# Kernel tuning notes

Hardware: AMD Instinct MI355X
Metric: run time of the kernel (lower is better)

## Reference

```python
import jax, jax.numpy as jnp
import numpy as np

EMBED_DIM = 1024
HEAD_DIM = 64


def setup_inputs() -> dict:
    key = jax.random.key(0)
    ks = jax.random.split(key, 7)
    B, S = 4, 2048
    s = 1.0 / np.sqrt(EMBED_DIM)
    h = jax.random.normal(ks[0], (B, S, EMBED_DIM), dtype=jnp.float32)
    Wq = jax.random.normal(ks[1], (EMBED_DIM, HEAD_DIM), dtype=jnp.float32) * s
    bq = jax.random.normal(ks[2], (HEAD_DIM,), dtype=jnp.float32) * 0.01
    Wk = jax.random.normal(ks[3], (EMBED_DIM, HEAD_DIM), dtype=jnp.float32) * s
    bk = jax.random.normal(ks[4], (HEAD_DIM,), dtype=jnp.float32) * 0.01
    Wv = jax.random.normal(ks[5], (EMBED_DIM, HEAD_DIM), dtype=jnp.float32) * s
    bv = jax.random.normal(ks[6], (HEAD_DIM,), dtype=jnp.float32) * 0.01
    return {"h": h, "Wq": Wq, "bq": bq, "Wk": Wk, "bk": bk, "Wv": Wv, "bv": bv}


def reference(h, Wq, bq, Wk, bk, Wv, bv):
    # Linear projections: h [B,S,E] -> q,k [B,S,D]
    q = jnp.einsum("bse,ed->bsd", h, Wq) + bq
    k = jnp.einsum("bse,ed->bsd", h, Wk) + bk
    v = jnp.einsum("bse,ed->bsd", h, Wv) + bv  # computed but UNUSED (faithful to source)
    del v
    scale = 1.0 / jnp.sqrt(jnp.asarray(HEAD_DIM, dtype=q.dtype))
    # scores [B, Sq, Sk]
    scores = jnp.einsum("bqd,bkd->bqk", q, k) * scale
    # NOTE: source uses softmax over dim=1 (query axis), not the key axis
    weights = jax.nn.softmax(scores, axis=1)
    # NOTE: source passes h (not v) as the value tensor
    out = jnp.einsum("bqk,bke->bqe", weights, h)  # [B, Sq, E]
    return out
```

## Files before the change

### kernel.cpp

```cpp
#include <hip/hip_runtime.h>
#include <hip/hip_bf16.h>
#include <math.h>

#define EMBED 1024
#define HDIM  64
#define BATCH 4
#define SEQ   2048

typedef __attribute__((ext_vector_type(8))) short short8;
typedef __attribute__((ext_vector_type(4))) float f32x4;
typedef unsigned int u32;
typedef unsigned short u16;

static __device__ __forceinline__ u16 f2bf(float f) {
    union { float f; u32 u; } v; v.f = f;
    u32 r = v.u + 0x7fffu + ((v.u >> 16) & 1u);
    return (u16)(r >> 16);
}

static __device__ __forceinline__ void gload_lds16(const u16* g, u16* l) {
    __builtin_amdgcn_global_load_lds(
        (const __attribute__((address_space(1))) u32*)g,
        (__attribute__((address_space(3))) u32*)l, 16, 0, 0);
}

__global__ __launch_bounds__(256) void wt_kernel(
    const float* __restrict__ Wq, const float* __restrict__ Wk,
    u16* __restrict__ WqT, u16* __restrict__ WkT)
{
    __shared__ float tile[64][65];
    const float* W = blockIdx.y ? Wk : Wq;
    u16* WT = blockIdx.y ? WkT : WqT;
    int e0 = blockIdx.x * 64;
    int t = threadIdx.x, c = t & 63, r4 = t >> 6;
    for (int r = r4; r < 64; r += 4)
        tile[r][c] = W[(size_t)(e0 + r) * HDIM + c];
    __syncthreads();
    for (int d = r4; d < 64; d += 4)
        WT[(size_t)d * EMBED + e0 + c] = f2bf(tile[c][d]);
}

__global__ __launch_bounds__(256) void proj_kernel(
    const float* __restrict__ h, const u16* __restrict__ WqT, const u16* __restrict__ WkT,
    const float* __restrict__ bq, const float* __restrict__ bk,
    u16* __restrict__ Qbf, u16* __restrict__ Kbf)
{
    __shared__ u16 hs[2][16][136];
    int b = blockIdx.x >> 7, s0 = (blockIdx.x & 127) * 16;
    int t = threadIdx.x, lane = t & 63, w = t >> 6;
    int l15 = lane & 15, quad = lane >> 4;
    int pj = w >> 1, nh = (w & 1) * 32;
    const float* hb = h + ((size_t)b * SEQ + s0) * EMBED;
    const u16* Wp = pj ? WkT : WqT;
    int r = t >> 4, c4 = (t & 15) * 4;

    f32x4 preA0 = *(const f32x4*)(hb + (size_t)r * EMBED + c4);
    f32x4 preA1 = *(const f32x4*)(hb + (size_t)r * EMBED + 64 + c4);
    f32x4 preB0 = *(const f32x4*)(hb + (size_t)r * EMBED + 128 + c4);
    f32x4 preB1 = *(const f32x4*)(hb + (size_t)r * EMBED + 192 + c4);
    f32x4 accA[2], accB[2];
    accA[0] = accA[1] = accB[0] = accB[1] = (f32x4){0.f, 0.f, 0.f, 0.f};

    const u16* Wrow0 = Wp + (size_t)(nh + l15) * EMBED;
    const u16* Wrow1 = Wp + (size_t)(nh + 16 + l15) * EMBED;

    short8 cw[8];
#pragma unroll
    for (int i = 0; i < 4; i++) {
        cw[i]     = *(const short8*)(Wrow0 + i * 32 + quad * 8);
        cw[4 + i] = *(const short8*)(Wrow1 + i * 32 + quad * 8);
    }

    for (int it = 0; it < 8; ++it) {
        int ec = it * 128, buf = it & 1;
        uint2 pk;
        pk.x = (u32)f2bf(preA0[0]) | ((u32)f2bf(preA0[1]) << 16);
        pk.y = (u32)f2bf(preA0[2]) | ((u32)f2bf(preA0[3]) << 16);
        *(uint2*)&hs[buf][r][c4] = pk;
        pk.x = (u32)f2bf(preA1[0]) | ((u32)f2bf(preA1[1]) << 16);
        pk.y = (u32)f2bf(preA1[2]) | ((u32)f2bf(preA1[3]) << 16);
        *(uint2*)&hs[buf][r][64 + c4] = pk;
        __syncthreads();

        preA0 = preB0; preA1 = preB1;
        if (it + 2 < 8) {
            preB0 = *(const f32x4*)(hb + (size_t)r * EMBED + ec + 256 + c4);
            preB1 = *(const f32x4*)(hb + (size_t)r * EMBED + ec + 320 + c4);
        }
        short8 nw[8];
#pragma unroll
        for (int i = 0; i < 8; i++) nw[i] = cw[i];
        if (it + 1 < 8) {
#pragma unroll
            for (int i = 0; i < 4; i++) {
                nw[i]     = *(const short8*)(Wrow0 + ec + 128 + i * 32 + quad * 8);
                nw[4 + i] = *(const short8*)(Wrow1 + ec + 128 + i * 32 + quad * 8);
            }
        }

        short8 a0 = *(const short8*)&hs[buf][l15][quad * 8];
        short8 a1 = *(const short8*)&hs[buf][l15][32 + quad * 8];
        short8 a2 = *(const short8*)&hs[buf][l15][64 + quad * 8];
        short8 a3 = *(const short8*)&hs[buf][l15][96 + quad * 8];
        accA[0] = __builtin_amdgcn_mfma_f32_16x16x32_bf16(a0, cw[0], accA[0], 0, 0, 0);
        accA[1] = __builtin_amdgcn_mfma_f32_16x16x32_bf16(a0, cw[4], accA[1], 0, 0, 0);
        accB[0] = __builtin_amdgcn_mfma_f32_16x16x32_bf16(a1, cw[1], accB[0], 0, 0, 0);
        accB[1] = __builtin_amdgcn_mfma_f32_16x16x32_bf16(a1, cw[5], accB[1], 0, 0, 0);
        accA[0] = __builtin_amdgcn_mfma_f32_16x16x32_bf16(a2, cw[2], accA[0], 0, 0, 0);
        accA[1] = __builtin_amdgcn_mfma_f32_16x16x32_bf16(a2, cw[6], accA[1], 0, 0, 0);
        accB[0] = __builtin_amdgcn_mfma_f32_16x16x32_bf16(a3, cw[3], accB[0], 0, 0, 0);
        accB[1] = __builtin_amdgcn_mfma_f32_16x16x32_bf16(a3, cw[7], accB[1], 0, 0, 0);
#pragma unroll
        for (int i = 0; i < 8; i++) cw[i] = nw[i];
    }

    const float* bias = pj ? bk : bq;
    float scale = pj ? 1.0f : 0.125f;
    u16* outp = pj ? Kbf : Qbf;
    float bv0 = bias[nh + l15], bv1 = bias[nh + 16 + l15];
#pragma unroll
    for (int rr = 0; rr < 4; rr++) {
        size_t row = (size_t)b * SEQ + s0 + quad * 4 + rr;
        outp[row * HDIM + nh + l15]      = f2bf((accA[0][rr] + accB[0][rr] + bv0) * scale);
        outp[row * HDIM + nh + 16 + l15] = f2bf((accA[1][rr] + accB[1][rr] + bv1) * scale);
    }
}

__global__ __launch_bounds__(512) void sw_kernel(
    const u16* __restrict__ Qbf, const u16* __restrict__ Kbf,
    u16* __restrict__ Wmat, float* __restrict__ invl)
{
    __shared__ float sl[8][64];
    int b = blockIdx.y;
    int k0 = blockIdx.x * 64;
    int t = threadIdx.x, lane = t & 63, w = t >> 6;
    int l15 = lane & 15, quad = lane >> 4;
    const u16* Qb = Qbf + (size_t)b * SEQ * HDIM;
    const u16* Kb = Kbf + (size_t)b * SEQ * HDIM;
    u16* Wb = Wmat + (size_t)b * SEQ * SEQ;

    short8 kfr[4][2];
#pragma unroll
    for (int g = 0; g < 4; g++)
#pragma unroll
        for (int hh = 0; hh < 2; hh++)
            kfr[g][hh] = *(const short8*)(
                Kb + (size_t)(k0 + g * 16 + l15) * HDIM + hh * 32 + quad * 8);

    f32x4 lacc[4];
#pragma unroll
    for (int g = 0; g < 4; g++) lacc[g] = (f32x4){0.f, 0.f, 0.f, 0.f};

    int qs = w * 256;
    short8 cf[2][2];
#pragma unroll
    for (int a = 0; a < 2; a++)
#pragma unroll
        for (int hh = 0; hh < 2; hh++)
            cf[a][hh] = *(const short8*)(
                Qb + (size_t)(qs + a * 16 + l15) * HDIM + hh * 32 + quad * 8);

    for (int q0 = qs; q0 < qs + 256; q0 += 32) {
        short8 nf[2][2];
#pragma unroll
        for (int a = 0; a < 2; a++)
#pragma unroll
            for (int hh = 0; hh < 2; hh++) nf[a][hh] = cf[a][hh];
        if (q0 + 32 < qs + 256) {
#pragma unroll
            for (int a = 0; a < 2; a++)
#pragma unroll
                for (int hh = 0; hh < 2; hh++)
                    nf[a][hh] = *(const short8*)(
                        Qb + (size_t)(q0 + 32 + a * 16 + l15) * HDIM + hh * 32 + quad * 8);
        }
        f32x4 acc[2][4];
#pragma unroll
        for (int a = 0; a < 2; a++)
#pragma unroll
            for (int g = 0; g < 4; g++) acc[a][g] = (f32x4){0.f, 0.f, 0.f, 0.f};
#pragma unroll
        for (int a = 0; a < 2; a++)
#pragma unroll
            for (int g = 0; g < 4; g++) {
                acc[a][g] = __builtin_amdgcn_mfma_f32_16x16x32_bf16(
                    kfr[g][0], cf[a][0], acc[a][g], 0, 0, 0);
                acc[a][g] = __builtin_amdgcn_mfma_f32_16x16x32_bf16(
                    kfr[g][1], cf[a][1], acc[a][g], 0, 0, 0);
            }
#pragma unroll
        for (int a = 0; a < 2; a++) {
            u16* wrow = Wb + (size_t)(q0 + a * 16 + l15) * SEQ + k0;
#pragma unroll
            for (int g = 0; g < 4; g++) {
                float e0 = __expf(acc[a][g][0]), e1 = __expf(acc[a][g][1]);
                float e2 = __expf(acc[a][g][2]), e3 = __expf(acc[a][g][3]);
                lacc[g][0] += e0; lacc[g][1] += e1;
                lacc[g][2] += e2; lacc[g][3] += e3;
                uint2 pk;
                pk.x = (u32)f2bf(e0) | ((u32)f2bf(e1) << 16);
                pk.y = (u32)f2bf(e2) | ((u32)f2bf(e3) << 16);
                *(uint2*)(wrow + g * 16 + quad * 4) = pk;
            }
        }
#pragma unroll
        for (int a = 0; a < 2; a++)
#pragma unroll
            for (int hh = 0; hh < 2; hh++) cf[a][hh] = nf[a][hh];
    }
#pragma unroll
    for (int m = 1; m <= 8; m <<= 1)
#pragma unroll
        for (int g = 0; g < 4; g++) {
            lacc[g][0] += __shfl_xor(lacc[g][0], m, 64);
            lacc[g][1] += __shfl_xor(lacc[g][1], m, 64);
            lacc[g][2] += __shfl_xor(lacc[g][2], m, 64);
            lacc[g][3] += __shfl_xor(lacc[g][3], m, 64);
        }
    if (l15 == 0) {
#pragma unroll
        for (int g = 0; g < 4; g++) {
            sl[w][g * 16 + quad * 4 + 0] = lacc[g][0];
            sl[w][g * 16 + quad * 4 + 1] = lacc[g][1];
            sl[w][g * 16 + quad * 4 + 2] = lacc[g][2];
            sl[w][g * 16 + quad * 4 + 3] = lacc[g][3];
        }
    }
    __syncthreads();
    if (t < 64) {
        float s = ((sl[0][t] + sl[1][t]) + (sl[2][t] + sl[3][t]))
                + ((sl[4][t] + sl[5][t]) + (sl[6][t] + sl[7][t]));
        invl[b * SEQ + k0 + t] = 1.0f / s;
    }
}

__global__ __launch_bounds__(256) void tscale_kernel(
    const float* __restrict__ h, const float* __restrict__ invl,
    u16* __restrict__ hT)
{
    __shared__ float tile[64][65];
    int b  = blockIdx.z;
    int s0 = blockIdx.x * 64, e0 = blockIdx.y * 64;
    int t = threadIdx.x;
    int r16 = t >> 4, c4 = (t & 15) * 4;
    const float* hb = h + (size_t)b * SEQ * EMBED;
#pragma unroll
    for (int rr = r16; rr < 64; rr += 16) {
        f32x4 v = *(const f32x4*)(hb + (size_t)(s0 + rr) * EMBED + e0 + c4);
        *(f32x4*)&tile[rr][c4] = v;
    }
    __syncthreads();
    f32x4 il4 = *(const f32x4*)(invl + b * SEQ + s0 + c4);
    u16* hTb = hT + (size_t)b * EMBED * SEQ;
#pragma unroll
    for (int er = r16; er < 64; er += 16) {
        u16 p0 = f2bf(tile[c4 + 0][er] * il4[0]);
        u16 p1 = f2bf(tile[c4 + 1][er] * il4[1]);
        u16 p2 = f2bf(tile[c4 + 2][er] * il4[2]);
        u16 p3 = f2bf(tile[c4 + 3][er] * il4[3]);
        uint2 pk;
        pk.x = (u32)p0 | ((u32)p1 << 16);
        pk.y = (u32)p2 | ((u32)p3 << 16);
        *(uint2*)(hTb + (size_t)(e0 + er) * SEQ + s0 + c4) = pk;
    }
}

__global__ __launch_bounds__(512, 2) void out_gemm_kernel(
    const u16* __restrict__ Wmat, const u16* __restrict__ hT, float* __restrict__ out)
{
    __shared__ __align__(16) char smem[3 * 49152];
    int b = blockIdx.z;
    int q0 = blockIdx.x * 256, e0 = blockIdx.y * 128;
    int t = threadIdx.x, lane = t & 63, w = t >> 6;
    int l15 = lane & 15, quad = lane >> 4;
    const u16* Wb  = Wmat + (size_t)b * SEQ * SEQ;
    const u16* hTb = hT + (size_t)b * EMBED * SEQ;
    int kf = w >> 2;
    int wm = (w >> 1) & 1, wn = w & 1;
    int wq = wm * 128, we = wn * 64;

    f32x4 acc[8][4];
#pragma unroll
    for (int i = 0; i < 8; i++)
#pragma unroll
        for (int j = 0; j < 4; j++) acc[i][j] = (f32x4){0.f, 0.f, 0.f, 0.f};

    int st_rl = lane >> 3;
    int st_pc = lane & 7;

    const u16* gA[4];
    const u16* gB[2];
#pragma unroll
    for (int ld = 0; ld < 4; ld++) {
        int row = w * 32 + ld * 8 + st_rl;
        int cg  = st_pc ^ (row & 7);
        gA[ld] = Wb + (size_t)(q0 + row) * SEQ + cg * 8;
    }
#pragma unroll
    for (int ld = 0; ld < 2; ld++) {
        int row = w * 16 + ld * 8 + st_rl;
        int cg  = st_pc ^ (row & 7);
        gB[ld] = hTb + (size_t)(e0 + row) * SEQ + cg * 8;
    }
    int dA[4], dB[2];
#pragma unroll
    for (int ld = 0; ld < 4; ld++) dA[ld] = (w * 32 + ld * 8) * 128 + lane * 16;
#pragma unroll
    for (int ld = 0; ld < 2; ld++) dB[ld] = 32768 + (w * 16 + ld * 8) * 128 + lane * 16;
    int offA[8], offB[4];
#pragma unroll
    for (int ii = 0; ii < 8; ii++) {
        int ra  = wq + ii * 16 + l15;
        int pca = (kf * 4 + quad) ^ (ra & 7);
        offA[ii] = ra * 128 + pca * 16;
    }
#pragma unroll
    for (int j = 0; j < 4; j++) {
        int rb  = we + j * 16 + l15;
        int pcb = (kf * 4 + quad) ^ (rb & 7);
        offB[j] = 32768 + rb * 128 + pcb * 16;
    }

#define STAGE_H1(si)                                                           \
    {                                                                          \
        gload_lds16(gA[0], (u16*)(smem + (si) * 49152 + dA[0]));               \
        gload_lds16(gA[1], (u16*)(smem + (si) * 49152 + dA[1]));               \
        gload_lds16(gB[0], (u16*)(smem + (si) * 49152 + dB[0]));               \
    }
#define STAGE_H2(si)                                                           \
    {                                                                          \
        gload_lds16(gA[2], (u16*)(smem + (si) * 49152 + dA[2]));               \
        gload_lds16(gA[3], (u16*)(smem + (si) * 49152 + dA[3]));               \
        gload_lds16(gB[1], (u16*)(smem + (si) * 49152 + dB[1]));               \
    }
#define ADV()                                                                  \
    {                                                                          \
        gA[0] += 64; gA[1] += 64; gA[2] += 64; gA[3] += 64;                    \
        gB[0] += 64; gB[1] += 64;                                              \
    }

#define MFMA16(i0)                                                             \
    {                                                                          \
        _Pragma("unroll")                                                      \
        for (int ii = 0; ii < 4; ii++)                                         \
            _Pragma("unroll")                                                  \
            for (int j = 0; j < 4; j++)                                        \
                acc[(i0) + ii][j] = __builtin_amdgcn_mfma_f32_16x16x32_bf16(   \
                    af[ii], bfr[j], acc[(i0) + ii][j], 0, 0, 0);               \
    }

#define TILE(si, si2, DO_STAGE, VMC)                                           \
    {                                                                          \
        const char* Sb = smem + (si) * 49152;                                  \
        short8 af[4], bfr[4];                                                  \
                                                                  \
        _Pragma("unroll")                                                      \
        for (int ii = 0; ii < 4; ii++)                                         \
            af[ii] = *(const short8*)(Sb + offA[ii]);                          \
        _Pragma("unroll")                                                      \
        for (int j = 0; j < 4; j++)                                            \
            bfr[j] = *(const short8*)(Sb + offB[j]);                           \
        if (DO_STAGE) STAGE_H1(si2)                                            \
        __builtin_amdgcn_s_barrier();                                          \
        asm volatile("s_waitcnt lgkmcnt(0)" ::: "memory");                     \
        __builtin_amdgcn_sched_barrier(0);                                     \
        __builtin_amdgcn_s_setprio(1);                                         \
        MFMA16(0)                                                              \
        __builtin_amdgcn_s_setprio(0);                                         \
        __builtin_amdgcn_s_barrier();                                          \
                                                                  \
        _Pragma("unroll")                                                      \
        for (int ii = 0; ii < 4; ii++)                                         \
            af[ii] = *(const short8*)(Sb + offA[4 + ii]);                      \
        if (DO_STAGE) { STAGE_H2(si2) ADV() }                                  \
        __builtin_amdgcn_s_barrier();                                          \
        asm volatile("s_waitcnt lgkmcnt(0)" ::: "memory");                     \
        __builtin_amdgcn_sched_barrier(0);                                     \
        __builtin_amdgcn_s_setprio(1);                                         \
        MFMA16(4)                                                              \
        __builtin_amdgcn_s_setprio(0);                                         \
        if ((VMC) == 6) { asm volatile("s_waitcnt vmcnt(6)" ::: "memory"); }   \
        else if ((VMC) == 0) { asm volatile("s_waitcnt vmcnt(0)" ::: "memory"); } \
        __builtin_amdgcn_s_barrier();                                          \
    }

    STAGE_H1(0) STAGE_H2(0) ADV()
    STAGE_H1(1) STAGE_H2(1) ADV()
    asm volatile("s_waitcnt vmcnt(6)" ::: "memory");
    __builtin_amdgcn_s_barrier();

    for (int g = 0; g < 10; ++g) {
        TILE(0, 2, true, 6)
        TILE(1, 0, true, 6)
        TILE(2, 1, true, 6)
    }
    TILE(0, 2, false, 0)
    TILE(1, 0, false, -1)
#undef TILE
#undef STAGE_H1
#undef STAGE_H2
#undef ADV
#undef MFMA16

    float* red = (float*)smem;
    if (w >= 4) {
        float* reg = red + (size_t)(w & 3) * 8192;
#pragma unroll
        for (int i = 0; i < 8; i++)
#pragma unroll
            for (int j = 0; j < 4; j++)
                *(f32x4*)(reg + ((i * 4 + j) * 64 + lane) * 4) = acc[i][j];
    }
    __syncthreads();
    if (w < 4) {
        float* reg = red + (size_t)w * 8192;
        float* outb = out + (size_t)b * SEQ * EMBED;
#pragma unroll
        for (int i = 0; i < 8; i++)
#pragma unroll
            for (int j = 0; j < 4; j++) {
                f32x4 o = *(const f32x4*)(reg + ((i * 4 + j) * 64 + lane) * 4);
                o += acc[i][j];
#pragma unroll
                for (int r = 0; r < 4; r++)
                    outb[(size_t)(q0 + wq + i * 16 + quad * 4 + r) * EMBED
                         + e0 + we + j * 16 + l15] = o[r];
            }
    }
}

extern "C" void kernel_launch(void* const* d_in, const int* in_sizes, int n_in,
                              void* d_out, int out_size, void* d_ws, size_t ws_size,
                              hipStream_t stream) {
    (void)in_sizes; (void)n_in; (void)out_size; (void)ws_size;
    const float* h  = (const float*)d_in[0];
    const float* Wq = (const float*)d_in[1];
    const float* bq = (const float*)d_in[2];
    const float* Wk = (const float*)d_in[3];
    const float* bk = (const float*)d_in[4];
    float* out = (float*)d_out;

    char* ws = (char*)d_ws;
    u16*   Qbf  = (u16*)(ws);
    u16*   Kbf  = (u16*)(ws + (1ull << 20));
    u16*   hT   = (u16*)(ws + (2ull << 20));
    float* invl = (float*)(ws + (18ull << 20));
    u16*   WqT  = (u16*)(ws + (18ull << 20) + (128ull << 10));
    u16*   WkT  = (u16*)(ws + (18ull << 20) + (256ull << 10));
    u16*   Wmat = (u16*)(ws + (19ull << 20));

    hipLaunchKernelGGL(wt_kernel, dim3(16, 2), dim3(256), 0, stream, Wq, Wk, WqT, WkT);
    hipLaunchKernelGGL(proj_kernel, dim3(512), dim3(256), 0, stream,
                       h, WqT, WkT, bq, bk, Qbf, Kbf);
    hipLaunchKernelGGL(sw_kernel, dim3(32, 4), dim3(512), 0, stream,
                       Qbf, Kbf, Wmat, invl);
    hipLaunchKernelGGL(tscale_kernel, dim3(32, 16, 4), dim3(256), 0, stream,
                       h, invl, hT);
    hipLaunchKernelGGL(out_gemm_kernel, dim3(8, 8, 4), dim3(512), 0, stream,
                       Wmat, hT, out);
}
```

Baseline: 177.6 us.

## Split score-softmax kernel across query chunks with atomic column-sum reduction

The sw_kernel grid grows from 128 to 512 blocks by giving each block a quarter of the query range. Per-key exp sums are now combined across blocks with global atomicAdd into a buffer that wt_kernel zeroes first, and tscale_kernel takes the reciprocal itself. This targets under-occupancy: the old 128-block grid with long serial loops left most of the GPU's CUs idle. In exchange it adds atomic traffic, drops the Q-fragment prefetch, and makes the float summation order nondeterministic.

```diff
diff --git a/kernel.cpp b/kernel.cpp
--- a/kernel.cpp
+++ b/kernel.cpp
@@ -26,13 +26,14 @@
 
 __global__ __launch_bounds__(256) void wt_kernel(
     const float* __restrict__ Wq, const float* __restrict__ Wk,
-    u16* __restrict__ WqT, u16* __restrict__ WkT)
+    u16* __restrict__ WqT, u16* __restrict__ WkT, float* __restrict__ lsum)
 {
     __shared__ float tile[64][65];
     const float* W = blockIdx.y ? Wk : Wq;
     u16* WT = blockIdx.y ? WkT : WqT;
     int e0 = blockIdx.x * 64;
     int t = threadIdx.x, c = t & 63, r4 = t >> 6;
+    lsum[(blockIdx.y * 16 + blockIdx.x) * 256 + t] = 0.f;
     for (int r = r4; r < 64; r += 4)
         tile[r][c] = W[(size_t)(e0 + r) * HDIM + c];
     __syncthreads();
@@ -128,10 +129,9 @@
 
 __global__ __launch_bounds__(512) void sw_kernel(
     const u16* __restrict__ Qbf, const u16* __restrict__ Kbf,
-    u16* __restrict__ Wmat, float* __restrict__ invl)
+    u16* __restrict__ Wmat, float* __restrict__ lsum)
 {
-    __shared__ float sl[8][64];
-    int b = blockIdx.y;
+    int b = blockIdx.z;
     int k0 = blockIdx.x * 64;
     int t = threadIdx.x, lane = t & 63, w = t >> 6;
     int l15 = lane & 15, quad = lane >> 4;
@@ -151,29 +151,19 @@
 #pragma unroll
     for (int g = 0; g < 4; g++) lacc[g] = (f32x4){0.f, 0.f, 0.f, 0.f};
 
-    int qs = w * 256;
-    short8 cf[2][2];
-#pragma unroll
-    for (int a = 0; a < 2; a++)
-#pragma unroll
-        for (int hh = 0; hh < 2; hh++)
-            cf[a][hh] = *(const short8*)(
-                Qb + (size_t)(qs + a * 16 + l15) * HDIM + hh * 32 + quad * 8);
-
-    for (int q0 = qs; q0 < qs + 256; q0 += 32) {
-        short8 nf[2][2];
+    int qs = (blockIdx.y * 8 + w) * 64;
+
+#pragma unroll
+    for (int half = 0; half < 2; ++half) {
+        int q0 = qs + half * 32;
+        short8 cf[2][2];
 #pragma unroll
         for (int a = 0; a < 2; a++)
 #pragma unroll
-            for (int hh = 0; hh < 2; hh++) nf[a][hh] = cf[a][hh];
-        if (q0 + 32 < qs + 256) {
-#pragma unroll
-            for (int a = 0; a < 2; a++)
-#pragma unroll
-                for (int hh = 0; hh < 2; hh++)
-                    nf[a][hh] = *(const short8*)(
-                        Qb + (size_t)(q0 + 32 + a * 16 + l15) * HDIM + hh * 32 + quad * 8);
-        }
+            for (int hh = 0; hh < 2; hh++)
+                cf[a][hh] = *(const short8*)(
+                    Qb + (size_t)(q0 + a * 16 + l15) * HDIM + hh * 32 + quad * 8);
+
         f32x4 acc[2][4];
 #pragma unroll
         for (int a = 0; a < 2; a++)
@@ -203,10 +193,6 @@
                 *(uint2*)(wrow + g * 16 + quad * 4) = pk;
             }
         }
-#pragma unroll
-        for (int a = 0; a < 2; a++)
-#pragma unroll
-            for (int hh = 0; hh < 2; hh++) cf[a][hh] = nf[a][hh];
     }
 #pragma unroll
     for (int m = 1; m <= 8; m <<= 1)
@@ -218,24 +204,19 @@
             lacc[g][3] += __shfl_xor(lacc[g][3], m, 64);
         }
     if (l15 == 0) {
+        float* lp = lsum + b * SEQ + k0 + quad * 4;
 #pragma unroll
         for (int g = 0; g < 4; g++) {
-            sl[w][g * 16 + quad * 4 + 0] = lacc[g][0];
-            sl[w][g * 16 + quad * 4 + 1] = lacc[g][1];
-            sl[w][g * 16 + quad * 4 + 2] = lacc[g][2];
-            sl[w][g * 16 + quad * 4 + 3] = lacc[g][3];
+            atomicAdd(lp + g * 16 + 0, lacc[g][0]);
+            atomicAdd(lp + g * 16 + 1, lacc[g][1]);
+            atomicAdd(lp + g * 16 + 2, lacc[g][2]);
+            atomicAdd(lp + g * 16 + 3, lacc[g][3]);
         }
     }
-    __syncthreads();
-    if (t < 64) {
-        float s = ((sl[0][t] + sl[1][t]) + (sl[2][t] + sl[3][t]))
-                + ((sl[4][t] + sl[5][t]) + (sl[6][t] + sl[7][t]));
-        invl[b * SEQ + k0 + t] = 1.0f / s;
-    }
 }
 
 __global__ __launch_bounds__(256) void tscale_kernel(
-    const float* __restrict__ h, const float* __restrict__ invl,
+    const float* __restrict__ h, const float* __restrict__ lsum,
     u16* __restrict__ hT)
 {
     __shared__ float tile[64][65];
@@ -250,7 +231,12 @@
         *(f32x4*)&tile[rr][c4] = v;
     }
     __syncthreads();
-    f32x4 il4 = *(const f32x4*)(invl + b * SEQ + s0 + c4);
+    f32x4 ls = *(const f32x4*)(lsum + b * SEQ + s0 + c4);
+    f32x4 il4;
+    il4[0] = __builtin_amdgcn_rcpf(ls[0]);
+    il4[1] = __builtin_amdgcn_rcpf(ls[1]);
+    il4[2] = __builtin_amdgcn_rcpf(ls[2]);
+    il4[3] = __builtin_amdgcn_rcpf(ls[3]);
     u16* hTb = hT + (size_t)b * EMBED * SEQ;
 #pragma unroll
     for (int er = r16; er < 64; er += 16) {
@@ -444,18 +430,19 @@
     u16*   Qbf  = (u16*)(ws);
     u16*   Kbf  = (u16*)(ws + (1ull << 20));
     u16*   hT   = (u16*)(ws + (2ull << 20));
-    float* invl = (float*)(ws + (18ull << 20));
+    float* lsum = (float*)(ws + (18ull << 20));
     u16*   WqT  = (u16*)(ws + (18ull << 20) + (128ull << 10));
     u16*   WkT  = (u16*)(ws + (18ull << 20) + (256ull << 10));
     u16*   Wmat = (u16*)(ws + (19ull << 20));
 
-    hipLaunchKernelGGL(wt_kernel, dim3(16, 2), dim3(256), 0, stream, Wq, Wk, WqT, WkT);
+    hipLaunchKernelGGL(wt_kernel, dim3(16, 2), dim3(256), 0, stream,
+                       Wq, Wk, WqT, WkT, lsum);
     hipLaunchKernelGGL(proj_kernel, dim3(512), dim3(256), 0, stream,
                        h, WqT, WkT, bq, bk, Qbf, Kbf);
-    hipLaunchKernelGGL(sw_kernel, dim3(32, 4), dim3(512), 0, stream,
-                       Qbf, Kbf, Wmat, invl);
+    hipLaunchKernelGGL(sw_kernel, dim3(32, 4, 4), dim3(512), 0, stream,
+                       Qbf, Kbf, Wmat, lsum);
     hipLaunchKernelGGL(tscale_kernel, dim3(32, 16, 4), dim3(256), 0, stream,
-                       h, invl, hT);
+                       h, lsum, hT);
     hipLaunchKernelGGL(out_gemm_kernel, dim3(8, 8, 4), dim3(512), 0, stream,
                        Wmat, hT, out);
 }
```

After: 171.8 us. 3.2% less time.
